# Kernel optimization log

Hardware: AMD Instinct MI355X
Metric: run time of the kernel (lower is better)

## Reference

```python
import jax, jax.numpy as jnp
import numpy as np

DIM, E, H, HS = 2048, 8, 1408, 2816
B, S = 4, 2048


def setup_inputs() -> dict:
    key = jax.random.key(0)
    ks = jax.random.split(key, 12)
    sc = 0.02
    return {
        "x": jax.random.normal(ks[0], (B, S, DIM), jnp.float32),
        "gate_w": jax.random.normal(ks[1], (E, DIM), jnp.float32) * sc,
        "gate_b": jnp.zeros((E,), jnp.float32),
        "w1": jax.random.normal(ks[2], (E, H, DIM), jnp.float32) * sc,
        "b1": jnp.zeros((E, H), jnp.float32),
        "w3": jax.random.normal(ks[3], (E, H, DIM), jnp.float32) * sc,
        "b3": jnp.zeros((E, H), jnp.float32),
        "w2": jax.random.normal(ks[4], (E, DIM, H), jnp.float32) * sc,
        "b2": jnp.zeros((E, DIM), jnp.float32),
        "sh_gate": jax.random.normal(ks[5], (HS, DIM), jnp.float32) * sc,
        "sh_up": jax.random.normal(ks[6], (HS, DIM), jnp.float32) * sc,
        "sh_down": jax.random.normal(ks[7], (DIM, HS), jnp.float32) * sc,
        "top_k": 2,
    }


def reference(x, gate_w, gate_b, w1, b1, w3, b3, w2, b2, sh_gate, sh_up, sh_down, top_k):
    shape = x.shape
    xt = x.reshape(-1, DIM)                       # [T, D]
    T = xt.shape[0]

    # Router: softmax -> top-k (bias is None so gathered weights == topk probs)
    logits = xt @ gate_w.T + gate_b               # [T, E]
    scores = jax.nn.softmax(logits, axis=-1)
    topk_w, topk_idx = jax.lax.top_k(scores, top_k)  # [T, K]
    # combine weights per (token, expert); topk indices are distinct per row
    combine = jnp.zeros((T, E), xt.dtype).at[jnp.arange(T)[:, None], topk_idx].add(topk_w)

    # Routed experts: dense batched SwiGLU over all experts, weighted combine.
    g = jax.nn.silu(jnp.einsum("td,ehd->teh", xt, w1) + b1)  # [T, E, H]
    u = jnp.einsum("td,ehd->teh", xt, w3) + b3               # [T, E, H]
    hw = (g * u) * combine[:, :, None]                        # weight before down-proj
    routed = jnp.einsum("teh,edh->td", hw, w2) + combine @ b2  # [T, D]

    # Shared expert (bias-free SwiGLU)
    shared = (jax.nn.silu(xt @ sh_gate.T) * (xt @ sh_up.T)) @ sh_down.T

    return (shared + routed).reshape(shape)
```

## Files before the change

### kernel.cpp

```cpp
#include <hip/hip_runtime.h>
#include <stdint.h>

#define DIM  2048
#define NEXP 8
#define NH   1408
#define NHS  2816
#define NT   8192
#define NA   (NT*2)

typedef unsigned short u16;
typedef short bf16x8 __attribute__((ext_vector_type(8)));
typedef float f32x4 __attribute__((ext_vector_type(4)));

typedef __attribute__((address_space(1))) const uint32_t gas_u32;
typedef __attribute__((address_space(3))) uint32_t las_u32;

__device__ __forceinline__ u16 f2bf(float f) {
  uint32_t x = __builtin_bit_cast(uint32_t, f);
  x += 0x7FFFu + ((x >> 16) & 1u);
  return (u16)(x >> 16);
}

__device__ __forceinline__ void gload_lds16(const void* g, void* l) {
  __builtin_amdgcn_global_load_lds((gas_u32*)g, (las_u32*)l, 16, 0, 0);
}

struct alignas(16) US8 { u16 u[8]; };
struct alignas(8)  US4 { u16 u[4]; };

__global__ __launch_bounds__(256) void convert_kernel(const float* __restrict__ src,
                                                      u16* __restrict__ dst, int n8) {
  int i = blockIdx.x * 256 + threadIdx.x;
  if (i >= n8) return;
  const float4* s = (const float4*)src + (size_t)i * 2;
  float4 a = s[0], b = s[1];
  US8 r;
  r.u[0]=f2bf(a.x); r.u[1]=f2bf(a.y); r.u[2]=f2bf(a.z); r.u[3]=f2bf(a.w);
  r.u[4]=f2bf(b.x); r.u[5]=f2bf(b.y); r.u[6]=f2bf(b.z); r.u[7]=f2bf(b.w);
  *((US8*)dst + i) = r;
}

__global__ __launch_bounds__(256) void convert_ilv(const float* __restrict__ src,
                                                   u16* __restrict__ dst, int n8, int par) {
  int i = blockIdx.x * 256 + threadIdx.x;
  if (i >= n8) return;
  int row = i >> 8, c = i & 255;
  const float4* s = (const float4*)src + (size_t)i * 2;
  float4 a = s[0], b = s[1];
  US8 r;
  r.u[0]=f2bf(a.x); r.u[1]=f2bf(a.y); r.u[2]=f2bf(a.z); r.u[3]=f2bf(a.w);
  r.u[4]=f2bf(b.x); r.u[5]=f2bf(b.y); r.u[6]=f2bf(b.z); r.u[7]=f2bf(b.w);
  *((US8*)dst + (((size_t)(2*row + par)) << 8) + c) = r;
}

__global__ void zero_counts(int* counts) { if (threadIdx.x < NEXP) counts[threadIdx.x] = 0; }

__global__ __launch_bounds__(64) void router_kernel(const float* __restrict__ x,
    const float* __restrict__ gw, const float* __restrict__ gb,
    u16* __restrict__ xb,
    int* __restrict__ tope, float* __restrict__ topw, int* __restrict__ counts) {
  const int t = blockIdx.x;
  const int lane = threadIdx.x;
  const float4* xr = (const float4*)(x + (size_t)t * DIM);
  float4 xv[8];
  #pragma unroll
  for (int j = 0; j < 8; j++) xv[j] = xr[j * 64 + lane];
  US4* xrow = (US4*)(xb + (size_t)t * DIM);
  #pragma unroll
  for (int j = 0; j < 8; j++) {
    US4 r4;
    r4.u[0] = f2bf(xv[j].x); r4.u[1] = f2bf(xv[j].y);
    r4.u[2] = f2bf(xv[j].z); r4.u[3] = f2bf(xv[j].w);
    xrow[j * 64 + lane] = r4;
  }
  float p[NEXP];
  #pragma unroll
  for (int e = 0; e < NEXP; e++) {
    const float4* gr = (const float4*)(gw + (size_t)e * DIM);
    float s = 0.f;
    #pragma unroll
    for (int j = 0; j < 8; j++) {
      float4 g = gr[j * 64 + lane];
      s += xv[j].x*g.x + xv[j].y*g.y + xv[j].z*g.z + xv[j].w*g.w;
    }
    p[e] = s;
  }
  #pragma unroll
  for (int off = 32; off > 0; off >>= 1) {
    #pragma unroll
    for (int e = 0; e < NEXP; e++) p[e] += __shfl_xor(p[e], off);
  }
  if (lane == 0) {
    float pr[NEXP];
    float mx = -1e30f;
    #pragma unroll
    for (int e = 0; e < NEXP; e++) { p[e] += gb[e]; mx = fmaxf(mx, p[e]); }
    float den = 0.f;
    #pragma unroll
    for (int e = 0; e < NEXP; e++) { pr[e] = __expf(p[e] - mx); den += pr[e]; }
    float inv = 1.f / den;
    #pragma unroll
    for (int e = 0; e < NEXP; e++) pr[e] *= inv;
    int e0 = 0;
    #pragma unroll
    for (int e = 1; e < NEXP; e++) if (pr[e] > pr[e0]) e0 = e;
    int e1 = (e0 == 0) ? 1 : 0;
    #pragma unroll
    for (int e = 0; e < NEXP; e++) { if (e != e0 && pr[e] > pr[e1]) e1 = e; }
    tope[t*2]   = e0; tope[t*2+1] = e1;
    topw[t*2]   = pr[e0]; topw[t*2+1] = pr[e1];
    atomicAdd(&counts[e0], 1); atomicAdd(&counts[e1], 1);
  }
}

__global__ void scan_kernel(const int* __restrict__ counts, int* __restrict__ offsets,
                            int* __restrict__ cursor) {
  if (threadIdx.x == 0) {
    int s = 0;
    for (int e = 0; e < NEXP; e++) { offsets[e] = s; cursor[e] = s; s += counts[e]; }
    offsets[NEXP] = s;
  }
}

__global__ __launch_bounds__(256) void assign_kernel(const int* __restrict__ tope,
    const float* __restrict__ topw, int* __restrict__ cursor,
    int* __restrict__ ptok, float* __restrict__ pw) {
  int t = blockIdx.x * 256 + threadIdx.x;
  if (t >= NT) return;
  #pragma unroll
  for (int k = 0; k < 2; k++) {
    int e = tope[t*2+k];
    int pos = atomicAdd(&cursor[e], 1);
    ptok[pos] = t;
    pw[pos]   = topw[t*2+k];
  }
}

#define BAR() { asm volatile("" ::: "memory"); __builtin_amdgcn_s_barrier(); asm volatile("" ::: "memory"); }
#define VM6 asm volatile("s_waitcnt vmcnt(6)" ::: "memory")
#define VM0 asm volatile("s_waitcnt vmcnt(0)" ::: "memory")

template<int EPI>
__global__ __launch_bounds__(512, 2) void gemm8(
    const u16* __restrict__ A, const u16* __restrict__ Bw, u16* __restrict__ Hout,
    const float* __restrict__ biasG, const float* __restrict__ biasU,
    const int* __restrict__ offsets, const int* __restrict__ ptok,
    const float* __restrict__ pw, int M, int N, int K, int Hf)
{
  constexpr bool SEG = (EPI == 1);
  extern __shared__ char smem[];
  const int nt = blockIdx.x, mt = blockIdx.y;
  int e = 0, seg = 0, cnt = M;
  if (SEG) { e = blockIdx.z; seg = offsets[e]; cnt = offsets[e+1] - seg; if (mt*256 >= cnt) return; }
  const int tid = threadIdx.x, wave = tid >> 6, lane = tid & 63;
  const int NKT = K >> 6;

  const u16* Bp = Bw + (SEG ? (size_t)e * (size_t)N * K : (size_t)0);
  const u16* sAp[2][2]; const u16* sBp[2][2];
  {
    const int trow = tid >> 3;
    const int tch  = (tid & 7) ^ (trow & 7);
    #pragma unroll
    for (int h = 0; h < 2; h++)
      #pragma unroll
      for (int j = 0; j < 2; j++) {
        int r = mt*256 + h*128 + j*64 + trow;
        if (SEG) r = (r < cnt) ? r : (cnt - 1);
        size_t arow = SEG ? (size_t)ptok[seg + r] : (size_t)r;
        sAp[h][j] = A + arow * (size_t)K + tch * 8;
        int br = nt*256 + h*128 + j*64 + trow;
        sBp[h][j] = Bp + (size_t)br * K + tch * 8;
      }
  }

  const int wm = wave >> 2, wn = wave & 3, hb = wn >> 1;
  const int ln15 = lane & 15, kg = lane >> 4;
  const int c0 = (kg ^ (ln15 & 7)) << 4;
  const char* Ab0 = smem + ((0*2 + wm) << 14);
  const char* Ab1 = smem + ((1*2 + wm) << 14);
  const char* Bb0 = smem + 65536 + ((0*2 + hb) << 14);
  const char* Bb1 = smem + 65536 + ((1*2 + hb) << 14);
  const int arow0 = ln15 * 128;
  const int brow0 = ((wn & 1) * 64 + ln15) * 128;

  f32x4 acc[8][4];
  #pragma unroll
  for (int m = 0; m < 8; m++)
    #pragma unroll
    for (int n = 0; n < 4; n++) acc[m][n] = (f32x4){0,0,0,0};

  bf16x8 fa[4][2], fb[4][2];

#define STA(buf,h,kt) { size_t k_ = (size_t)(kt) * 64; \
  gload_lds16(sAp[h][0] + k_, smem + (((buf)*2+(h))<<14) + wave*1024); \
  gload_lds16(sAp[h][1] + k_, smem + (((buf)*2+(h))<<14) + 8192 + wave*1024); }
#define STB(buf,h,kt) { size_t k_ = (size_t)(kt) * 64; \
  gload_lds16(sBp[h][0] + k_, smem + 65536 + (((buf)*2+(h))<<14) + wave*1024); \
  gload_lds16(sBp[h][1] + k_, smem + 65536 + (((buf)*2+(h))<<14) + 8192 + wave*1024); }
#define LDFA(AB, qm) { _Pragma("unroll") for (int m_ = 0; m_ < 4; m_++) { \
  const char* p_ = (AB) + (qm)*8192 + m_*2048 + arow0; \
  fa[m_][0] = *(const bf16x8*)(p_ + c0); fa[m_][1] = *(const bf16x8*)(p_ + (c0 ^ 64)); } }
#define LDFB(BB) { _Pragma("unroll") for (int n_ = 0; n_ < 4; n_++) { \
  const char* p_ = (BB) + n_*2048 + brow0; \
  fb[n_][0] = *(const bf16x8*)(p_ + c0); fb[n_][1] = *(const bf16x8*)(p_ + (c0 ^ 64)); } }
#define PH(qm, n0) { __builtin_amdgcn_s_setprio(1); \
  _Pragma("unroll") for (int kk_ = 0; kk_ < 2; kk_++) \
  _Pragma("unroll") for (int m_ = 0; m_ < 4; m_++) \
  _Pragma("unroll") for (int n_ = 0; n_ < 2; n_++) \
    acc[(qm)*4+m_][(n0)+n_] = __builtin_amdgcn_mfma_f32_16x16x32_bf16( \
        fa[m_][kk_], fb[(n0)+n_][kk_], acc[(qm)*4+m_][(n0)+n_], 0, 0, 0); \
  __builtin_amdgcn_s_setprio(0); }

  STB(0,0,0); STB(0,1,0); STA(0,0,0); STA(0,1,0);
  STB(1,0,1); STB(1,1,1); STA(1,0,1);
  VM6; BAR();

  for (int t = 0; t < NKT; t += 2) {
    const bool last = (t + 2 >= NKT);
    LDFB(Bb0); LDFA(Ab0, 0);
    STA(1,1,t+1);
    PH(0,0);
    BAR();
    if (!last) STB(0,0,t+2);
    PH(0,2);
    BAR();
    LDFA(Ab0, 1);
    if (!last) STB(0,1,t+2);
    PH(1,2);
    BAR();
    if (!last) { STA(0,0,t+2); VM6; } else { VM0; }
    PH(1,0);
    BAR();
    LDFB(Bb1); LDFA(Ab1, 0);
    if (!last) STA(0,1,t+2);
    PH(0,0);
    BAR();
    if (!last) STB(1,0,t+3);
    PH(0,2);
    BAR();
    LDFA(Ab1, 1);
    if (!last) STB(1,1,t+3);
    PH(1,2);
    BAR();
    if (!last) { STA(1,0,t+3); VM6; }
    PH(1,0);
    BAR();
  }

  #pragma unroll
  for (int mi = 0; mi < 8; mi++) {
    #pragma unroll
    for (int ni = 0; ni < 4; ni++) {
      int colC = nt*256 + wn*64 + ni*16 + ln15;
      int h = colC >> 1;
      int par = ln15 & 1;
      #pragma unroll
      for (int i = 0; i < 4; i++) {
        float v = acc[mi][ni][i];
        float v2 = __shfl_xor(v, 1);
        float g = par ? v2 : v;
        float uu = par ? v : v2;
        int rr = mt*256 + wm*128 + mi*16 + kg*4 + i;
        if (EPI == 1) { g += biasG[e*Hf + h]; uu += biasU[e*Hf + h]; }
        float hv = (g / (1.f + __expf(-g))) * uu;
        if (EPI == 0) {
          if (par == 0) Hout[(size_t)rr * Hf + h] = f2bf(hv);
        } else {
          if (par == 0 && rr < cnt) {
            int ai = seg + rr;
            Hout[(size_t)ai * Hf + h] = f2bf(hv * pw[ai]);
          }
        }
      }
    }
  }
#undef STA
#undef STB
#undef LDFA
#undef LDFB
#undef PH
}

template<bool ROUTED>
__global__ __launch_bounds__(256, 2) void gemm_down(
    const u16* __restrict__ Hin, const u16* __restrict__ W,
    const float* __restrict__ B2, float* __restrict__ Out,
    const int* __restrict__ offsets, const int* __restrict__ ptok,
    const float* __restrict__ pw, int Kdim)
{
  const int nt = blockIdx.x;
  const int mt = blockIdx.y;
  int e = 0, seg = 0, cnt = NT;
  if (ROUTED) {
    e = blockIdx.z;
    seg = offsets[e];
    cnt = offsets[e+1] - seg;
    if (mt * 128 >= cnt) return;
  }
  const int m0 = mt * 128;
  const int tid = threadIdx.x;
  const int wave = tid >> 6, lane = tid & 63;

  __shared__ u16 sA[128*64];
  __shared__ u16 sB[128*64];
  char* sAc = (char*)sA;
  char* sBc = (char*)sB;

  const u16* aSrc[4]; const u16* bSrc[4];
  #pragma unroll
  for (int j = 0; j < 4; j++) {
    int c = j * 256 + tid;
    int row = c >> 3, gch = (c & 7) ^ (row & 7);
    int r = m0 + row;
    size_t arow;
    if (ROUTED) { r = (r < cnt) ? r : (cnt - 1); arow = (size_t)(seg + r); }
    else        { arow = (size_t)r; }
    aSrc[j] = Hin + arow * (size_t)Kdim + gch * 8;
    size_t brow = (size_t)(ROUTED ? e * DIM : 0) + nt * 128 + row;
    bSrc[j] = W + brow * (size_t)Kdim + gch * 8;
  }

  f32x4 acc[4][4];
  #pragma unroll
  for (int m = 0; m < 4; m++)
    #pragma unroll
    for (int n = 0; n < 4; n++) acc[m][n] = (f32x4){0,0,0,0};

  const int wr = (wave >> 1) * 64, wc = (wave & 1) * 64;
  const int lr = lane & 15, kg = lane >> 4;
  int aOff[4], bOff[4];
  #pragma unroll
  for (int m = 0; m < 4; m++) { int row = wr + m*16 + lr; aOff[m] = row*128 + ((kg ^ (row & 7)) & 7) * 16; }
  #pragma unroll
  for (int n = 0; n < 4; n++) { int row = wc + n*16 + lr; bOff[n] = row*128 + ((kg ^ (row & 7)) & 7) * 16; }

  for (int k0 = 0; k0 < Kdim; k0 += 64) {
    __syncthreads();
    #pragma unroll
    for (int j = 0; j < 4; j++) {
      gload_lds16(aSrc[j] + k0, sAc + j*4096 + wave*1024);
      gload_lds16(bSrc[j] + k0, sBc + j*4096 + wave*1024);
    }
    __syncthreads();
    bf16x8 af[4][2], bf[4][2];
    #pragma unroll
    for (int m = 0; m < 4; m++) {
      af[m][0] = *(const bf16x8*)(sAc + aOff[m]);
      af[m][1] = *(const bf16x8*)(sAc + (aOff[m] ^ 64));
    }
    #pragma unroll
    for (int n = 0; n < 4; n++) {
      bf[n][0] = *(const bf16x8*)(sBc + bOff[n]);
      bf[n][1] = *(const bf16x8*)(sBc + (bOff[n] ^ 64));
    }
    #pragma unroll
    for (int kk = 0; kk < 2; kk++)
      #pragma unroll
      for (int m = 0; m < 4; m++)
        #pragma unroll
        for (int n = 0; n < 4; n++)
          acc[m][n] = __builtin_amdgcn_mfma_f32_16x16x32_bf16(af[m][kk], bf[n][kk], acc[m][n], 0, 0, 0);
  }

  const int col0 = nt * 128 + wc;
  #pragma unroll
  for (int m = 0; m < 4; m++) {
    #pragma unroll
    for (int n = 0; n < 4; n++) {
      #pragma unroll
      for (int i = 0; i < 4; i++) {
        int rl = wr + m*16 + (lane >> 4) * 4 + i;
        int gr = m0 + rl;
        int col = col0 + n*16 + (lane & 15);
        float v = acc[m][n][i];
        if (ROUTED) {
          if (gr < cnt) {
            int ai = seg + gr;
            int token = ptok[ai];
            float w = pw[ai];
            atomicAdd(Out + (size_t)token * DIM + col, v + w * B2[e * DIM + col]);
          }
        } else {
          Out[(size_t)gr * DIM + col] = v;
        }
      }
    }
  }
}

extern "C" void kernel_launch(void* const* d_in, const int* in_sizes, int n_in,
                              void* d_out, int out_size, void* d_ws, size_t ws_size,
                              hipStream_t stream) {
  (void)in_sizes; (void)n_in; (void)out_size; (void)ws_size;
  const float* x      = (const float*)d_in[0];
  const float* gate_w = (const float*)d_in[1];
  const float* gate_b = (const float*)d_in[2];
  const float* w1     = (const float*)d_in[3];
  const float* b1     = (const float*)d_in[4];
  const float* w3     = (const float*)d_in[5];
  const float* b3     = (const float*)d_in[6];
  const float* w2     = (const float*)d_in[7];
  const float* b2     = (const float*)d_in[8];
  const float* shg    = (const float*)d_in[9];
  const float* shu    = (const float*)d_in[10];
  const float* shd    = (const float*)d_in[11];
  float* out = (float*)d_out;

  char* ws = (char*)d_ws;
  size_t off = 0;
  auto alloc = [&](size_t bytes) -> void* {
    void* p = ws + off;
    off += (bytes + 255) & ~(size_t)255;
    return p;
  };
  u16* xb    = (u16*)alloc((size_t)NT * DIM * 2);
  u16* wupr  = (u16*)alloc((size_t)NEXP * 2 * NH * DIM * 2);
  u16* w2b   = (u16*)alloc((size_t)NEXP * DIM * NH * 2);
  u16* wupsh = (u16*)alloc((size_t)2 * NHS * DIM * 2);
  u16* shdb  = (u16*)alloc((size_t)DIM * NHS * 2);
  u16* hsh   = (u16*)alloc((size_t)NT * NHS * 2);
  u16* hr    = (u16*)alloc((size_t)NA * NH * 2);
  int*   tope    = (int*)alloc(NT * 2 * 4);
  float* topw    = (float*)alloc(NT * 2 * 4);
  int*   ptok    = (int*)alloc(NA * 4);
  float* pw      = (float*)alloc(NA * 4);
  int*   counts  = (int*)alloc(64);
  int*   offsets = (int*)alloc(64);
  int*   cursor  = (int*)alloc(64);

  (void)hipFuncSetAttribute((const void*)gemm8<0>, hipFuncAttributeMaxDynamicSharedMemorySize, 131072);
  (void)hipFuncSetAttribute((const void*)gemm8<1>, hipFuncAttributeMaxDynamicSharedMemorySize, 131072);

  auto cvt = [&](const float* s, u16* d, size_t n) {
    int n8 = (int)(n / 8);
    convert_kernel<<<(n8 + 255) / 256, 256, 0, stream>>>(s, d, n8);
  };
  auto cvi = [&](const float* s, u16* d, size_t n, int par) {
    int n8 = (int)(n / 8);
    convert_ilv<<<(n8 + 255) / 256, 256, 0, stream>>>(s, d, n8, par);
  };
  cvi(w1,  wupr,  (size_t)NEXP * NH * DIM, 0);
  cvi(w3,  wupr,  (size_t)NEXP * NH * DIM, 1);
  cvt(w2,  w2b,   (size_t)NEXP * DIM * NH);
  cvi(shg, wupsh, (size_t)NHS * DIM, 0);
  cvi(shu, wupsh, (size_t)NHS * DIM, 1);
  cvt(shd, shdb,  (size_t)DIM * NHS);

  zero_counts<<<1, 64, 0, stream>>>(counts);
  router_kernel<<<NT, 64, 0, stream>>>(x, gate_w, gate_b, xb, tope, topw, counts);
  scan_kernel<<<1, 1, 0, stream>>>(counts, offsets, cursor);
  assign_kernel<<<NT / 256, 256, 0, stream>>>(tope, topw, cursor, ptok, pw);

  gemm8<0><<<dim3(2*NHS/256, NT/256, 1), 512, 131072, stream>>>(
      xb, wupsh, hsh, nullptr, nullptr, nullptr, nullptr, nullptr,
      NT, 2*NHS, DIM, NHS);
  gemm8<1><<<dim3(2*NH/256, NT/256, NEXP), 512, 131072, stream>>>(
      xb, wupr, hr, b1, b3, offsets, ptok, pw,
      NT, 2*NH, DIM, NH);
  gemm_down<false><<<dim3(DIM / 128, NT / 128, 1), 256, 0, stream>>>(
      hsh, shdb, nullptr, out, nullptr, nullptr, nullptr, NHS);
  gemm_down<true><<<dim3(DIM / 128, NT / 128, NEXP), 256, 0, stream>>>(
      hr, w2b, b2, out, offsets, ptok, pw, NH);
}
```

Before: 1.188 ms.

## Restructure gemm8 main loop into barrier-fenced MFMA phases with split B fragment loads

Replaces the PH/BAR phase macros in the gate/up GEMM main loop with an MFMA16 macro. Each phase now starts with a workgroup barrier, a full lgkmcnt(0) wait and a sched_barrier, and ends with a second barrier. B fragment LDS reads are split into two halves, so the second half is loaded after the first MFMA phase rather than all at once. An lgkmcnt(8) wait is added before the first phase. The aim is a tighter, compiler-proof interleaving of LDS reads, global-to-LDS copies and MFMA clusters across waves. In exchange it doubles the barriers per phase and forces full LDS-read drains before each MFMA block.

```diff
diff --git a/kernel.cpp b/kernel.cpp
--- a/kernel.cpp
+++ b/kernel.cpp
@@ -139,6 +139,7 @@
 #define BAR() { asm volatile("" ::: "memory"); __builtin_amdgcn_s_barrier(); asm volatile("" ::: "memory"); }
 #define VM6 asm volatile("s_waitcnt vmcnt(6)" ::: "memory")
 #define VM0 asm volatile("s_waitcnt vmcnt(0)" ::: "memory")
+#define LGKM8 asm volatile("s_waitcnt lgkmcnt(8)" ::: "memory")
 
 template<int EPI>
 __global__ __launch_bounds__(512, 2) void gemm8(
@@ -200,16 +201,24 @@
 #define LDFA(AB, qm) { _Pragma("unroll") for (int m_ = 0; m_ < 4; m_++) { \
   const char* p_ = (AB) + (qm)*8192 + m_*2048 + arow0; \
   fa[m_][0] = *(const bf16x8*)(p_ + c0); fa[m_][1] = *(const bf16x8*)(p_ + (c0 ^ 64)); } }
-#define LDFB(BB) { _Pragma("unroll") for (int n_ = 0; n_ < 4; n_++) { \
-  const char* p_ = (BB) + n_*2048 + brow0; \
-  fb[n_][0] = *(const bf16x8*)(p_ + c0); fb[n_][1] = *(const bf16x8*)(p_ + (c0 ^ 64)); } }
-#define PH(qm, n0) { __builtin_amdgcn_s_setprio(1); \
+#define LDFB2(BB, n0) { _Pragma("unroll") for (int n_ = 0; n_ < 2; n_++) { \
+  const char* p_ = (BB) + ((n0)+n_)*2048 + brow0; \
+  fb[(n0)+n_][0] = *(const bf16x8*)(p_ + c0); fb[(n0)+n_][1] = *(const bf16x8*)(p_ + (c0 ^ 64)); } }
+#define MFMA16(QM, N0) { \
+  asm volatile("" ::: "memory"); \
+  __builtin_amdgcn_s_barrier(); \
+  asm volatile("s_waitcnt lgkmcnt(0)" ::: "memory"); \
+  __builtin_amdgcn_sched_barrier(0); \
+  __builtin_amdgcn_s_setprio(1); \
   _Pragma("unroll") for (int kk_ = 0; kk_ < 2; kk_++) \
   _Pragma("unroll") for (int m_ = 0; m_ < 4; m_++) \
   _Pragma("unroll") for (int n_ = 0; n_ < 2; n_++) \
-    acc[(qm)*4+m_][(n0)+n_] = __builtin_amdgcn_mfma_f32_16x16x32_bf16( \
-        fa[m_][kk_], fb[(n0)+n_][kk_], acc[(qm)*4+m_][(n0)+n_], 0, 0, 0); \
-  __builtin_amdgcn_s_setprio(0); }
+    acc[(QM)*4+m_][(N0)+n_] = __builtin_amdgcn_mfma_f32_16x16x32_bf16( \
+        fa[m_][kk_], fb[(N0)+n_][kk_], acc[(QM)*4+m_][(N0)+n_], 0, 0, 0); \
+  __builtin_amdgcn_s_setprio(0); \
+  asm volatile("" ::: "memory"); \
+  __builtin_amdgcn_s_barrier(); \
+  asm volatile("" ::: "memory"); }
 
   STB(0,0,0); STB(0,1,0); STA(0,0,0); STA(0,1,0);
   STB(1,0,1); STB(1,1,1); STA(1,0,1);
@@ -217,34 +226,30 @@
 
   for (int t = 0; t < NKT; t += 2) {
     const bool last = (t + 2 >= NKT);
-    LDFB(Bb0); LDFA(Ab0, 0);
+    LDFB2(Bb0, 0); LDFA(Ab0, 0);
     STA(1,1,t+1);
-    PH(0,0);
-    BAR();
+    LGKM8;
+    MFMA16(0, 0);
+    LDFB2(Bb0, 2);
     if (!last) STB(0,0,t+2);
-    PH(0,2);
-    BAR();
+    MFMA16(0, 2);
     LDFA(Ab0, 1);
     if (!last) STB(0,1,t+2);
-    PH(1,2);
-    BAR();
+    MFMA16(1, 2);
     if (!last) { STA(0,0,t+2); VM6; } else { VM0; }
-    PH(1,0);
-    BAR();
-    LDFB(Bb1); LDFA(Ab1, 0);
+    MFMA16(1, 0);
+    LDFB2(Bb1, 0); LDFA(Ab1, 0);
     if (!last) STA(0,1,t+2);
-    PH(0,0);
-    BAR();
+    LGKM8;
+    MFMA16(0, 0);
+    LDFB2(Bb1, 2);
     if (!last) STB(1,0,t+3);
-    PH(0,2);
-    BAR();
+    MFMA16(0, 2);
     LDFA(Ab1, 1);
     if (!last) STB(1,1,t+3);
-    PH(1,2);
-    BAR();
+    MFMA16(1, 2);
     if (!last) { STA(1,0,t+3); VM6; }
-    PH(1,0);
-    BAR();
+    MFMA16(1, 0);
   }
 
   #pragma unroll
@@ -277,8 +282,8 @@
 #undef STA
 #undef STB
 #undef LDFA
-#undef LDFB
-#undef PH
+#undef LDFB2
+#undef MFMA16
 }
 
 template<bool ROUTED>
```

Result: slower. 1.213 ms (+2.2%).
